# Kernel tuning notes

Hardware: AMD Instinct MI355X
Metric: run time of the kernel (lower is better)

## Reference

```python
import jax, jax.numpy as jnp
import numpy as np

NODE, HID, B, T = 207, 16, 64, 12
HIDDEN_DIM = NODE * HID * 2  # 6624


def setup_inputs() -> dict:
    key = jax.random.key(0)
    ks = jax.random.split(key, 8)
    s = 0.02  # small init scale to keep tanh unsaturated
    return {
        "spline_vals": jax.random.normal(ks[0], (T, B, NODE, 2), jnp.float32),
        "init0": jax.random.normal(ks[1], (B, HIDDEN_DIM), jnp.float32),
        "Wf": jax.random.normal(ks[2], (HID, HID * 2), jnp.float32) * s,
        "bf": jnp.zeros((HID * 2,), jnp.float32),
        "Wg": jax.random.normal(ks[3], (HID, HID * HID), jnp.float32) * s,
        "bg": jnp.zeros((HID * HID,), jnp.float32),
        "conv_w": jax.random.normal(ks[4], (HID,), jnp.float32) * 0.1,
        "W_ih": jax.random.normal(ks[5], (HIDDEN_DIM, NODE * HID * 5), jnp.float32) * s,
        "b_ih": jnp.zeros((HIDDEN_DIM,), jnp.float32),
        "W_hh": jax.random.normal(ks[6], (HIDDEN_DIM, HIDDEN_DIM), jnp.float32) * s,
        "b_hh": jnp.zeros((HIDDEN_DIM,), jnp.float32),
    }


def reference(spline_vals, init0, Wf, bf, Wg, bg, conv_w, W_ih, b_ih, W_hh, b_hh):
    Tn, Bn, N, _ = spline_vals.shape
    H = Wf.shape[0]

    def rnn_seq(x):
        # torch nn.RNN on 2D input: unbatched sequence of length B, zero h0
        pre = x @ W_ih.T + b_ih  # (B, hidden_dim), batched GEMM up front

        def step(h, p):
            h = jnp.tanh(p + h @ W_hh.T + b_hh)
            return h, h

        _, hs = jax.lax.scan(step, jnp.zeros((W_hh.shape[0],), x.dtype), pre)
        return hs  # (B, hidden_dim)

    def outer(hz, sv):
        hzr = hz.reshape(Bn, N, H, 2)
        h, z = hzr[..., 0], hzr[..., 1]
        f = jnp.tanh(h @ Wf + bf).reshape(Bn, N, H, 2)      # func_f
        g = jnp.tanh(z @ Wg + bg).reshape(Bn, N, H, H)      # func_g
        fg = jnp.einsum('bnij,bnjk->bnik', g, f)            # (B,N,H,2)
        hz4 = jnp.stack([f, fg], axis=-1).reshape(Bn, N * H * 4)
        v = sv[..., 1]                                      # drop time channel -> (B,N)
        x = (conv_w[None, :, None] * v[:, None, :]).reshape(Bn, H * N)  # 1x1 conv
        inp = jnp.concatenate([x, hz4], axis=1)             # (B, N*H*5)
        hz_new = rnn_seq(inp)
        return hz_new, None

    hz, _ = jax.lax.scan(outer, init0, spline_vals)
    return hz
```

## Files before the change

### kernel.cpp

```cpp
#include <hip/hip_runtime.h>
#include <cstddef>
#include <cstdint>

#define NODE 207
#define HID 16
#define BATCH 64
#define TSTEPS 12
#define HIDDEN 6624
#define K_IH 16560
#define K_IH4 4140
#define H4 1656

__global__ __launch_bounds__(256) void build_inp_kernel(
    const float* __restrict__ spline,
    const float* __restrict__ hz,
    const float* __restrict__ Wf,
    const float* __restrict__ bf,
    const float* __restrict__ Wg,
    const float* __restrict__ bg,
    const float* __restrict__ conv_w,
    float* __restrict__ inpT,
    int t)
{
    const int bn = blockIdx.x;
    const int n = bn % NODE;
    const int b = bn / NODE;
    const int tid = threadIdx.x;

    __shared__ float shz[32];
    __shared__ float sf[32];
    __shared__ float sg[256];

    if (tid < 32) shz[tid] = hz[(size_t)b * HIDDEN + n * 32 + tid];
    __syncthreads();

    {
        float accg = bg[tid];
        #pragma unroll
        for (int i = 0; i < 16; ++i)
            accg = fmaf(shz[2 * i + 1], Wg[i * 256 + tid], accg);
        sg[tid] = tanhf(accg);
    }
    if (tid < 32) {
        float accf = bf[tid];
        #pragma unroll
        for (int i = 0; i < 16; ++i)
            accf = fmaf(shz[2 * i], Wf[i * 32 + tid], accf);
        float fv = tanhf(accf);
        sf[tid] = fv;
        int i2 = tid >> 1, kk = tid & 1;
        int kf = 3312 + n * 64 + i2 * 4 + kk * 2;
        inpT[(size_t)kf * 64 + b] = fv;
    } else if (tid < 48) {
        int i = tid - 32;
        float v = spline[((((size_t)t * BATCH + b) * NODE + n) * 2) + 1];
        inpT[(size_t)(i * NODE + n) * 64 + b] = conv_w[i] * v;
    }
    __syncthreads();
    if (tid < 32) {
        int i2 = tid >> 1, kk = tid & 1;
        float acc = 0.f;
        #pragma unroll
        for (int j = 0; j < 16; ++j)
            acc = fmaf(sg[i2 * 16 + j], sf[j * 2 + kk], acc);
        int kfg = 3312 + n * 64 + i2 * 4 + kk * 2 + 1;
        inpT[(size_t)kfg * 64 + b] = acc;
    }
}

__global__ __launch_bounds__(256) void gemm_ih_kernel(
    const float* __restrict__ Wih,
    const float* __restrict__ inpT,
    float* __restrict__ pre)
{
    const int jt = blockIdx.x >> 3;
    const int kc = blockIdx.x & 7;
    const int j0 = jt * 32;
    const int tid = threadIdx.x;
    const int b = tid & 63;
    const int p = __builtin_amdgcn_readfirstlane(tid >> 6);
    const int q = kc * 4 + p;

    float acc[32];
    #pragma unroll
    for (int jj = 0; jj < 32; ++jj) acc[jj] = 0.f;

    for (int g = q; g < K_IH4; g += 32) {
        const int k = g * 4;
        const float v0 = inpT[(size_t)(k + 0) * 64 + b];
        const float v1 = inpT[(size_t)(k + 1) * 64 + b];
        const float v2 = inpT[(size_t)(k + 2) * 64 + b];
        const float v3 = inpT[(size_t)(k + 3) * 64 + b];
        #pragma unroll
        for (int jj = 0; jj < 32; ++jj) {
            const float4 w = *reinterpret_cast<const float4*>(
                Wih + (size_t)(j0 + jj) * K_IH + k);
            acc[jj] = fmaf(w.x, v0, fmaf(w.y, v1, fmaf(w.z, v2, fmaf(w.w, v3, acc[jj]))));
        }
    }

    __shared__ float red[4][32][65];
    #pragma unroll
    for (int jj = 0; jj < 32; ++jj) red[p][jj][b] = acc[jj];
    __syncthreads();

    for (int idx = tid; idx < 2048; idx += 256) {
        const int jj = idx & 31;
        const int b2 = idx >> 5;
        const float s = red[0][jj][b2] + red[1][jj][b2] + red[2][jj][b2] + red[3][jj][b2];
        atomicAdd(pre + (size_t)b2 * HIDDEN + j0 + jj, s);
    }
}

__global__ __launch_bounds__(256) void rnn_kernel(
    const float* __restrict__ Whh,
    const float* __restrict__ b_hh,
    const float* __restrict__ b_ih,
    const float* __restrict__ pre,
    float* __restrict__ hz,
    unsigned int* __restrict__ bar,
    int bar_base)
{
    const int lane = threadIdx.x & 63;
    const int widx = threadIdx.x >> 6;
    const int gw = blockIdx.x * 4 + widx;
    const int nw = gridDim.x * 4;

    __shared__ float4 sh4[H4];
    const float4* W4 = reinterpret_cast<const float4*>(Whh);

    for (int b = 0; b < 64; ++b) {
        if (b > 0) {
            const float4* hrow = reinterpret_cast<const float4*>(hz + (size_t)(b - 1) * HIDDEN);
            for (int idx = threadIdx.x; idx < H4; idx += 256) sh4[idx] = hrow[idx];
        }
        __syncthreads();

        for (int j = gw; j < HIDDEN; j += nw) {
            float a0 = 0.f, a1 = 0.f, a2 = 0.f, a3 = 0.f;
            if (b > 0) {
                const float4* Wrow = W4 + (size_t)j * H4;
                #pragma unroll 5
                for (int it = 0; it < 25; ++it) {
                    const float4 w = Wrow[it * 64 + lane];
                    const float4 h = sh4[it * 64 + lane];
                    a0 = fmaf(w.x, h.x, a0);
                    a1 = fmaf(w.y, h.y, a1);
                    a2 = fmaf(w.z, h.z, a2);
                    a3 = fmaf(w.w, h.w, a3);
                }
                if (lane < 56) {
                    const float4 w = Wrow[1600 + lane];
                    const float4 h = sh4[1600 + lane];
                    a0 = fmaf(w.x, h.x, a0);
                    a1 = fmaf(w.y, h.y, a1);
                    a2 = fmaf(w.z, h.z, a2);
                    a3 = fmaf(w.w, h.w, a3);
                }
            }
            float acc = (a0 + a1) + (a2 + a3);
            #pragma unroll
            for (int off = 32; off > 0; off >>= 1) acc += __shfl_xor(acc, off, 64);
            if (lane == 0) {
                const float v = tanhf(pre[(size_t)b * HIDDEN + j] + acc + b_hh[j] + b_ih[j]);
                hz[(size_t)b * HIDDEN + j] = v;
            }
        }

        if (b != 63) {
            __syncthreads();
            if (threadIdx.x == 0) {
                __threadfence();
                __hip_atomic_fetch_add(bar, 1u, __ATOMIC_ACQ_REL, __HIP_MEMORY_SCOPE_AGENT);
                const unsigned int target =
                    (unsigned int)gridDim.x * (unsigned int)(bar_base + b + 1);
                while (__hip_atomic_load(bar, __ATOMIC_ACQUIRE, __HIP_MEMORY_SCOPE_AGENT) < target) {
                    __builtin_amdgcn_s_sleep(2);
                }
            }
            __syncthreads();
        }
    }
}

extern "C" void kernel_launch(void* const* d_in, const int* in_sizes, int n_in,
                              void* d_out, int out_size, void* d_ws, size_t ws_size,
                              hipStream_t stream)
{
    const float* spline = (const float*)d_in[0];
    const float* init0  = (const float*)d_in[1];
    const float* Wf     = (const float*)d_in[2];
    const float* bf     = (const float*)d_in[3];
    const float* Wg     = (const float*)d_in[4];
    const float* bg     = (const float*)d_in[5];
    const float* conv_w = (const float*)d_in[6];
    const float* Wih    = (const float*)d_in[7];
    const float* b_ih   = (const float*)d_in[8];
    const float* Whh    = (const float*)d_in[9];
    const float* b_hh   = (const float*)d_in[10];
    float* out = (float*)d_out;

    char* ws = (char*)d_ws;
    unsigned int* bar = (unsigned int*)ws;
    float* inpT  = (float*)(ws + 256);
    float* pre   = (float*)(ws + 256 + (size_t)K_IH * 64 * 4);
    float* hz_ws = (float*)(ws + 256 + (size_t)K_IH * 64 * 4
                                  + (size_t)BATCH * HIDDEN * 4);

    hipMemsetAsync(bar, 0, 256, stream);

    for (int t = 0; t < TSTEPS; ++t) {
        const float* hz_in = (t == 0) ? init0 : hz_ws;
        float* hz_out = (t == TSTEPS - 1) ? out : hz_ws;

        build_inp_kernel<<<BATCH * NODE, 256, 0, stream>>>(
            spline, hz_in, Wf, bf, Wg, bg, conv_w, inpT, t);

        hipMemsetAsync(pre, 0, (size_t)BATCH * HIDDEN * sizeof(float), stream);

        gemm_ih_kernel<<<207 * 8, 256, 0, stream>>>(Wih, inpT, pre);

        rnn_kernel<<<512, 256, 0, stream>>>(
            Whh, b_hh, b_ih, pre, hz_out, bar, t * 63);
    }
}
```

Before: 86.46 ms.

## Rework input GEMM tiling, widen RNN grid, and use hierarchical grid barrier

The input-projection GEMM now tiles K into LDS chunks with 16 output columns per block and writes two K-half partial results directly, which removes the memset and atomicAdds. The recurrent kernel runs 768 blocks with up to three rows per wave, reads h straight from global memory instead of staging it in LDS, and shares each h load across two rows. The single-counter grid barrier is replaced by 64 padded counters that one block aggregates before bumping a release counter, to reduce atomic contention on each of the 64 sequential steps. The risks are that 768 blocks must all be co-resident (launch bounds are raised to 3 blocks per SM) and that the extra barrier hop adds latency.

```diff
diff --git a/kernel.cpp b/kernel.cpp
--- a/kernel.cpp
+++ b/kernel.cpp
@@ -8,7 +8,6 @@
 #define TSTEPS 12
 #define HIDDEN 6624
 #define K_IH 16560
-#define K_IH4 4140
 #define H4 1656
 
 __global__ __launch_bounds__(256) void build_inp_kernel(
@@ -68,114 +67,172 @@
     }
 }
 
+#define KHALF 8280
+#define KC 36
+#define NCH 230
+
 __global__ __launch_bounds__(256) void gemm_ih_kernel(
     const float* __restrict__ Wih,
     const float* __restrict__ inpT,
-    float* __restrict__ pre)
-{
-    const int jt = blockIdx.x >> 3;
-    const int kc = blockIdx.x & 7;
-    const int j0 = jt * 32;
+    float* __restrict__ pre0,
+    float* __restrict__ pre1)
+{
+    const int jt = blockIdx.x >> 1;
+    const int kc = blockIdx.x & 1;
+    const int j0 = jt * 16;
     const int tid = threadIdx.x;
     const int b = tid & 63;
-    const int p = __builtin_amdgcn_readfirstlane(tid >> 6);
-    const int q = kc * 4 + p;
-
-    float acc[32];
-    #pragma unroll
-    for (int jj = 0; jj < 32; ++jj) acc[jj] = 0.f;
-
-    for (int g = q; g < K_IH4; g += 32) {
-        const int k = g * 4;
-        const float v0 = inpT[(size_t)(k + 0) * 64 + b];
-        const float v1 = inpT[(size_t)(k + 1) * 64 + b];
-        const float v2 = inpT[(size_t)(k + 2) * 64 + b];
-        const float v3 = inpT[(size_t)(k + 3) * 64 + b];
-        #pragma unroll
-        for (int jj = 0; jj < 32; ++jj) {
-            const float4 w = *reinterpret_cast<const float4*>(
-                Wih + (size_t)(j0 + jj) * K_IH + k);
-            acc[jj] = fmaf(w.x, v0, fmaf(w.y, v1, fmaf(w.z, v2, fmaf(w.w, v3, acc[jj]))));
-        }
-    }
-
-    __shared__ float red[4][32][65];
-    #pragma unroll
-    for (int jj = 0; jj < 32; ++jj) red[p][jj][b] = acc[jj];
-    __syncthreads();
-
-    for (int idx = tid; idx < 2048; idx += 256) {
-        const int jj = idx & 31;
-        const int b2 = idx >> 5;
-        const float s = red[0][jj][b2] + red[1][jj][b2] + red[2][jj][b2] + red[3][jj][b2];
-        atomicAdd(pre + (size_t)b2 * HIDDEN + j0 + jj, s);
-    }
-}
-
-__global__ __launch_bounds__(256) void rnn_kernel(
+    const int jg = tid >> 6;
+
+    __shared__ __align__(16) float s_inp[KC][64];
+    __shared__ __align__(16) float s_w[16][KC];
+
+    float acc[4] = {0.f, 0.f, 0.f, 0.f};
+
+    const int kbase = kc * KHALF;
+
+    for (int ch = 0; ch < NCH; ++ch) {
+        const int kb = kbase + ch * KC;
+        __syncthreads();
+        for (int idx = tid; idx < 576; idx += 256) {
+            const int k = idx >> 4;
+            const int c = (idx & 15) << 2;
+            *reinterpret_cast<float4*>(&s_inp[k][c]) =
+                *reinterpret_cast<const float4*>(inpT + (size_t)(kb + k) * 64 + c);
+        }
+        if (tid < 144) {
+            const int j = tid / 9;
+            const int c = (tid % 9) << 2;
+            *reinterpret_cast<float4*>(&s_w[j][c]) =
+                *reinterpret_cast<const float4*>(Wih + (size_t)(j0 + j) * K_IH + kb + c);
+        }
+        __syncthreads();
+
+        #pragma unroll
+        for (int kq = 0; kq < 9; ++kq) {
+            const float a0 = s_inp[kq * 4 + 0][b];
+            const float a1 = s_inp[kq * 4 + 1][b];
+            const float a2 = s_inp[kq * 4 + 2][b];
+            const float a3 = s_inp[kq * 4 + 3][b];
+            #pragma unroll
+            for (int q = 0; q < 4; ++q) {
+                const float4 w = *reinterpret_cast<const float4*>(&s_w[jg * 4 + q][kq * 4]);
+                acc[q] = fmaf(w.x, a0, fmaf(w.y, a1, fmaf(w.z, a2, fmaf(w.w, a3, acc[q]))));
+            }
+        }
+    }
+
+    float* preK = kc ? pre1 : pre0;
+    float4 r;
+    r.x = acc[0]; r.y = acc[1]; r.z = acc[2]; r.w = acc[3];
+    *reinterpret_cast<float4*>(preK + (size_t)b * HIDDEN + j0 + jg * 4) = r;
+}
+
+__global__ __launch_bounds__(256, 3) void rnn_kernel(
     const float* __restrict__ Whh,
     const float* __restrict__ b_hh,
     const float* __restrict__ b_ih,
-    const float* __restrict__ pre,
+    const float* __restrict__ pre0,
+    const float* __restrict__ pre1,
     float* __restrict__ hz,
-    unsigned int* __restrict__ bar,
+    unsigned int* __restrict__ barrier_mem,
     int bar_base)
 {
     const int lane = threadIdx.x & 63;
     const int widx = threadIdx.x >> 6;
     const int gw = blockIdx.x * 4 + widx;
-    const int nw = gridDim.x * 4;
-
-    __shared__ float4 sh4[H4];
+
+    const int j1 = gw;
+    const int j2 = gw + 3072;
+    const int j3 = gw + 6144;
+
     const float4* W4 = reinterpret_cast<const float4*>(Whh);
+    const float4* Wr1 = W4 + (size_t)j1 * H4;
+    const float4* Wr2 = W4 + (size_t)j2 * H4;
+    const float4* Wr3 = W4 + (size_t)j3 * H4;
 
     for (int b = 0; b < 64; ++b) {
+        float s1 = 0.f, s2 = 0.f, s3 = 0.f;
         if (b > 0) {
-            const float4* hrow = reinterpret_cast<const float4*>(hz + (size_t)(b - 1) * HIDDEN);
-            for (int idx = threadIdx.x; idx < H4; idx += 256) sh4[idx] = hrow[idx];
-        }
-        __syncthreads();
-
-        for (int j = gw; j < HIDDEN; j += nw) {
-            float a0 = 0.f, a1 = 0.f, a2 = 0.f, a3 = 0.f;
-            if (b > 0) {
-                const float4* Wrow = W4 + (size_t)j * H4;
-                #pragma unroll 5
+            const float4* h4 = reinterpret_cast<const float4*>(hz + (size_t)(b - 1) * HIDDEN);
+            float a1x = 0.f, a1y = 0.f, a1z = 0.f, a1w = 0.f;
+            float a2x = 0.f, a2y = 0.f, a2z = 0.f, a2w = 0.f;
+            #pragma unroll 8
+            for (int it = 0; it < 25; ++it) {
+                const float4 h = h4[it * 64 + lane];
+                const float4 w1 = Wr1[it * 64 + lane];
+                const float4 w2 = Wr2[it * 64 + lane];
+                a1x = fmaf(w1.x, h.x, a1x); a1y = fmaf(w1.y, h.y, a1y);
+                a1z = fmaf(w1.z, h.z, a1z); a1w = fmaf(w1.w, h.w, a1w);
+                a2x = fmaf(w2.x, h.x, a2x); a2y = fmaf(w2.y, h.y, a2y);
+                a2z = fmaf(w2.z, h.z, a2z); a2w = fmaf(w2.w, h.w, a2w);
+            }
+            if (lane < 56) {
+                const float4 h = h4[1600 + lane];
+                const float4 w1 = Wr1[1600 + lane];
+                const float4 w2 = Wr2[1600 + lane];
+                a1x = fmaf(w1.x, h.x, a1x); a1y = fmaf(w1.y, h.y, a1y);
+                a1z = fmaf(w1.z, h.z, a1z); a1w = fmaf(w1.w, h.w, a1w);
+                a2x = fmaf(w2.x, h.x, a2x); a2y = fmaf(w2.y, h.y, a2y);
+                a2z = fmaf(w2.z, h.z, a2z); a2w = fmaf(w2.w, h.w, a2w);
+            }
+            s1 = (a1x + a1y) + (a1z + a1w);
+            s2 = (a2x + a2y) + (a2z + a2w);
+            if (gw < 480) {
+                float cx = 0.f, cy = 0.f, cz = 0.f, cw = 0.f;
+                #pragma unroll 8
                 for (int it = 0; it < 25; ++it) {
-                    const float4 w = Wrow[it * 64 + lane];
-                    const float4 h = sh4[it * 64 + lane];
-                    a0 = fmaf(w.x, h.x, a0);
-                    a1 = fmaf(w.y, h.y, a1);
-                    a2 = fmaf(w.z, h.z, a2);
-                    a3 = fmaf(w.w, h.w, a3);
+                    const float4 h = h4[it * 64 + lane];
+                    const float4 w3 = Wr3[it * 64 + lane];
+                    cx = fmaf(w3.x, h.x, cx); cy = fmaf(w3.y, h.y, cy);
+                    cz = fmaf(w3.z, h.z, cz); cw = fmaf(w3.w, h.w, cw);
                 }
                 if (lane < 56) {
-                    const float4 w = Wrow[1600 + lane];
-                    const float4 h = sh4[1600 + lane];
-                    a0 = fmaf(w.x, h.x, a0);
-                    a1 = fmaf(w.y, h.y, a1);
-                    a2 = fmaf(w.z, h.z, a2);
-                    a3 = fmaf(w.w, h.w, a3);
-                }
-            }
-            float acc = (a0 + a1) + (a2 + a3);
-            #pragma unroll
-            for (int off = 32; off > 0; off >>= 1) acc += __shfl_xor(acc, off, 64);
-            if (lane == 0) {
-                const float v = tanhf(pre[(size_t)b * HIDDEN + j] + acc + b_hh[j] + b_ih[j]);
-                hz[(size_t)b * HIDDEN + j] = v;
-            }
+                    const float4 h = h4[1600 + lane];
+                    const float4 w3 = Wr3[1600 + lane];
+                    cx = fmaf(w3.x, h.x, cx); cy = fmaf(w3.y, h.y, cy);
+                    cz = fmaf(w3.z, h.z, cz); cw = fmaf(w3.w, h.w, cw);
+                }
+                s3 = (cx + cy) + (cz + cw);
+            }
+        }
+        #pragma unroll
+        for (int off = 32; off > 0; off >>= 1) {
+            s1 += __shfl_xor(s1, off, 64);
+            s2 += __shfl_xor(s2, off, 64);
+            s3 += __shfl_xor(s3, off, 64);
+        }
+        if (lane == 0) {
+            const size_t rb = (size_t)b * HIDDEN;
+            hz[rb + j1] = tanhf(pre0[rb + j1] + pre1[rb + j1] + b_hh[j1] + b_ih[j1] + s1);
+            hz[rb + j2] = tanhf(pre0[rb + j2] + pre1[rb + j2] + b_hh[j2] + b_ih[j2] + s2);
+            if (gw < 480)
+                hz[rb + j3] = tanhf(pre0[rb + j3] + pre1[rb + j3] + b_hh[j3] + b_ih[j3] + s3);
         }
 
         if (b != 63) {
+            const int gstep = bar_base + b;
             __syncthreads();
             if (threadIdx.x == 0) {
                 __threadfence();
-                __hip_atomic_fetch_add(bar, 1u, __ATOMIC_ACQ_REL, __HIP_MEMORY_SCOPE_AGENT);
-                const unsigned int target =
-                    (unsigned int)gridDim.x * (unsigned int)(bar_base + b + 1);
-                while (__hip_atomic_load(bar, __ATOMIC_ACQUIRE, __HIP_MEMORY_SCOPE_AGENT) < target) {
-                    __builtin_amdgcn_s_sleep(2);
+                __hip_atomic_fetch_add(barrier_mem + (size_t)(blockIdx.x & 63) * 16, 1u,
+                                       __ATOMIC_ACQ_REL, __HIP_MEMORY_SCOPE_AGENT);
+            }
+            if (blockIdx.x == 0 && threadIdx.x < 64) {
+                const unsigned int ltarget = 12u * (unsigned int)(gstep + 1);
+                while (__hip_atomic_load(barrier_mem + (size_t)threadIdx.x * 16,
+                                         __ATOMIC_ACQUIRE, __HIP_MEMORY_SCOPE_AGENT) < ltarget) {
+                    __builtin_amdgcn_s_sleep(1);
+                }
+                if (threadIdx.x == 0)
+                    __hip_atomic_fetch_add(barrier_mem + 1024, 1u,
+                                           __ATOMIC_ACQ_REL, __HIP_MEMORY_SCOPE_AGENT);
+            }
+            if (threadIdx.x == 0) {
+                const unsigned int etarget = (unsigned int)(gstep + 1);
+                while (__hip_atomic_load(barrier_mem + 1024,
+                                         __ATOMIC_ACQUIRE, __HIP_MEMORY_SCOPE_AGENT) < etarget) {
+                    __builtin_amdgcn_s_sleep(1);
                 }
             }
             __syncthreads();
@@ -202,12 +259,12 @@
 
     char* ws = (char*)d_ws;
     unsigned int* bar = (unsigned int*)ws;
-    float* inpT  = (float*)(ws + 256);
-    float* pre   = (float*)(ws + 256 + (size_t)K_IH * 64 * 4);
-    float* hz_ws = (float*)(ws + 256 + (size_t)K_IH * 64 * 4
-                                  + (size_t)BATCH * HIDDEN * 4);
-
-    hipMemsetAsync(bar, 0, 256, stream);
+    float* inpT = (float*)(ws + 8192);
+    float* pre0 = (float*)(ws + 8192 + 4239360);
+    float* pre1 = (float*)(ws + 8192 + 4239360 + 1695744);
+    float* hz_ws = (float*)(ws + 8192 + 4239360 + 2 * 1695744);
+
+    hipMemsetAsync(bar, 0, 8192, stream);
 
     for (int t = 0; t < TSTEPS; ++t) {
         const float* hz_in = (t == 0) ? init0 : hz_ws;
@@ -216,11 +273,9 @@
         build_inp_kernel<<<BATCH * NODE, 256, 0, stream>>>(
             spline, hz_in, Wf, bf, Wg, bg, conv_w, inpT, t);
 
-        hipMemsetAsync(pre, 0, (size_t)BATCH * HIDDEN * sizeof(float), stream);
-
-        gemm_ih_kernel<<<207 * 8, 256, 0, stream>>>(Wih, inpT, pre);
-
-        rnn_kernel<<<512, 256, 0, stream>>>(
-            Whh, b_hh, b_ih, pre, hz_out, bar, t * 63);
-    }
-}
+        gemm_ih_kernel<<<828, 256, 0, stream>>>(Wih, inpT, pre0, pre1);
+
+        rnn_kernel<<<768, 256, 0, stream>>>(
+            Whh, b_hh, b_ih, pre0, pre1, hz_out, bar, t * 63);
+    }
+}
```

Result: slower. 93.02 ms (+7.6%).
